# Performance work log

Hardware: AMD Instinct MI355X
Metric: run time of the kernel (lower is better)

The kernel has to match this reference:

```python
import jax, jax.numpy as jnp
import numpy as np

B, L, D, C, NB = 2, 256, 3, 256, 64
LN_EPS = 1e-5


def setup_inputs() -> dict:
    ks = jax.random.split(jax.random.key(0), 12)
    x_BLD = jax.random.normal(ks[0], (B, L, D), dtype=jnp.float32) * 0.5
    c_BD = jax.random.normal(ks[1], (B, C), dtype=jnp.float32)
    embed_w = jax.random.normal(ks[2], (NB, C), dtype=jnp.float32) * 0.02
    pos_w = jax.random.normal(ks[3], (128, C), dtype=jnp.float32) * 0.02
    bins = jnp.linspace(0.0, 3.0, NB - 1, dtype=jnp.float32)
    ada_w = jax.random.normal(ks[4], (3 * C, C), dtype=jnp.float32) * (C ** -0.5)
    ada_b = jnp.zeros((3 * C,), dtype=jnp.float32)
    ln_g = jnp.ones((C,), dtype=jnp.float32)
    ln_b = jnp.zeros((C,), dtype=jnp.float32)
    fc1_w = jax.random.normal(ks[5], (4 * C, C), dtype=jnp.float32) * (C ** -0.5)
    fc1_b = jnp.zeros((4 * C,), dtype=jnp.float32)
    fc2_w = jax.random.normal(ks[6], (C, 4 * C), dtype=jnp.float32) * ((4 * C) ** -0.5)
    fc2_b = jnp.zeros((C,), dtype=jnp.float32)
    return {"x_BLD": x_BLD, "c_BD": c_BD, "embed_w": embed_w, "pos_w": pos_w,
            "bins": bins, "ada_w": ada_w, "ada_b": ada_b, "ln_g": ln_g,
            "ln_b": ln_b, "fc1_w": fc1_w, "fc1_b": fc1_b, "fc2_w": fc2_w,
            "fc2_b": fc2_b}


def reference(x_BLD, c_BD, embed_w, pos_w, bins, ada_w, ada_b, ln_g, ln_b,
              fc1_w, fc1_b, fc2_w, fc2_b):
    # pairwise squared distances: [B, L, L]
    d_BLL = jnp.sum((x_BLD[:, :, None, :] - x_BLD[:, None, :, :]) ** 2, axis=-1)
    # bucketize (torch.bucketize right=False == searchsorted side='left')
    idx_BLL = jnp.searchsorted(bins, d_BLL, side="left")
    # relative position embedding: [L, L, C]
    rel = jnp.arange(L)[:, None] - jnp.arange(L)[None, :]
    rel = jnp.clip(rel, -64, 63) + 64
    pos_LLD = pos_w[rel]
    # adaLN modulation from conditioning: SiLU -> Linear -> 3 chunks
    mod = jax.nn.silu(c_BD) @ ada_w.T + ada_b            # [B, 3C]
    shift, scale, gate = jnp.split(mod, 3, axis=-1)      # each [B, C]
    shift = shift[:, None, None, :]
    scale = scale[:, None, None, :]
    gate = gate[:, None, None, :]
    # embed + pos, affine modulate
    s = embed_w[idx_BLL] + pos_LLD[None]                 # [B, L, L, C]
    s = s * (1.0 + scale) + shift
    # LayerNorm over channel dim
    mu = jnp.mean(s, axis=-1, keepdims=True)
    var = jnp.mean((s - mu) ** 2, axis=-1, keepdims=True)
    h = (s - mu) * jax.lax.rsqrt(var + LN_EPS) * ln_g + ln_b
    # MLP: Linear -> GELU(exact) -> Linear
    h = jax.nn.gelu(h @ fc1_w.T + fc1_b, approximate=False)
    h = h @ fc2_w.T + fc2_b
    return s + gate * h
```

## Files before the change

### kernel.cpp

```cpp
#include <hip/hip_runtime.h>
#include <math.h>

#define Cn 256
#define Ln 256
#define Bn 2
#define H1 1024
#define NIDX 64
#define NREL 128
#define NCOMBO 16384
#define TROWS 32

typedef __attribute__((ext_vector_type(8))) short bf16x8;
typedef __attribute__((ext_vector_type(4))) float f32x4;
typedef unsigned int u32;

__device__ __forceinline__ float gelu_exact(float x) {
    return 0.5f * x * (1.0f + erff(x * 0.70710678118654752f));
}
__device__ __forceinline__ short f2bf(float f) {
    unsigned u = __float_as_uint(f);
    return (short)((u + 0x7fffu + ((u >> 16) & 1u)) >> 16);
}

__global__ __launch_bounds__(256) void mod_kernel(
    const float* __restrict__ c_BD, const float* __restrict__ ada_w,
    const float* __restrict__ ada_b, float* __restrict__ mod)
{
    int o = blockIdx.x * 256 + threadIdx.x;
    int b = o / (3 * Cn);
    int j = o - b * (3 * Cn);
    const float* crow = c_BD + b * Cn;
    const float* wrow = ada_w + (size_t)j * Cn;
    float acc = 0.f;
    for (int k = 0; k < Cn; k += 4) {
        float4 cv = *(const float4*)(crow + k);
        float4 wv = *(const float4*)(wrow + k);
        acc += (cv.x / (1.f + expf(-cv.x))) * wv.x;
        acc += (cv.y / (1.f + expf(-cv.y))) * wv.y;
        acc += (cv.z / (1.f + expf(-cv.z))) * wv.z;
        acc += (cv.w / (1.f + expf(-cv.w))) * wv.w;
    }
    mod[o] = acc + ada_b[j];
}

__global__ __launch_bounds__(256) void cvt2_kernel(
    const float* __restrict__ s1, const float* __restrict__ s2,
    short* __restrict__ d1, short* __restrict__ d2)
{
    const int N = Cn * H1;
    int i = (blockIdx.x * 256 + threadIdx.x) * 4;
    const float* s;
    short* d;
    if (i < N) { s = s1 + i; d = d1 + i; }
    else       { s = s2 + (i - N); d = d2 + (i - N); }
    float4 v = *(const float4*)s;
    short4 o;
    o.x = f2bf(v.x); o.y = f2bf(v.y); o.z = f2bf(v.z); o.w = f2bf(v.w);
    *(short4*)d = o;
}

__global__ __launch_bounds__(256, 4) void table_fused_kernel(
    const float* __restrict__ embed_w, const float* __restrict__ pos_w,
    const float* __restrict__ ln_g, const float* __restrict__ ln_b,
    const short* __restrict__ fc1bf, const float* __restrict__ fc1_b,
    const short* __restrict__ fc2bf, const float* __restrict__ fc2_b,
    const float* __restrict__ mod, float* __restrict__ table)
{
    __shared__ __align__(16) short h_lds[TROWS][264];
    __shared__ __align__(16) short g_lds[TROWS][264];

    const int tid  = threadIdx.x;
    const int wave = tid >> 6;
    const int lane = tid & 63;
    const int quad = lane >> 4;
    const int l15  = lane & 15;

    const int base = blockIdx.x * TROWS;
    const int b    = base >> 13;
    const int idx  = (base >> 7) & 63;
    const int rel0 = base & 127;

    const float* modb = mod + b * (3 * Cn);
    const float* erow = embed_w + (size_t)idx * Cn;

    {
        const int c0 = lane * 4;
        float4 ev = *(const float4*)(erow + c0);
        float4 sc = *(const float4*)(modb + Cn + c0);
        sc.x += 1.f; sc.y += 1.f; sc.z += 1.f; sc.w += 1.f;
        const float4 sh = *(const float4*)(modb + c0);
        const float4 lg = *(const float4*)(ln_g + c0);
        const float4 lb = *(const float4*)(ln_b + c0);
        #pragma unroll
        for (int r8 = 0; r8 < 8; ++r8) {
            const int rr = wave * 8 + r8;
            const float4 p = *(const float4*)(pos_w + (size_t)(rel0 + rr) * Cn + c0);
            float v0 = (ev.x + p.x) * sc.x + sh.x;
            float v1 = (ev.y + p.y) * sc.y + sh.y;
            float v2 = (ev.z + p.z) * sc.z + sh.z;
            float v3 = (ev.w + p.w) * sc.w + sh.w;
            float sum = v0 + v1 + v2 + v3;
            #pragma unroll
            for (int off = 32; off; off >>= 1) sum += __shfl_xor(sum, off, 64);
            const float mu = sum * (1.f / Cn);
            float t0 = v0 - mu, t1 = v1 - mu, t2 = v2 - mu, t3 = v3 - mu;
            float p2 = t0 * t0 + t1 * t1 + t2 * t2 + t3 * t3;
            #pragma unroll
            for (int off = 32; off; off >>= 1) p2 += __shfl_xor(p2, off, 64);
            const float rstd = rsqrtf(p2 * (1.f / Cn) + 1e-5f);
            short4 hq;
            hq.x = f2bf(t0 * rstd * lg.x + lb.x);
            hq.y = f2bf(t1 * rstd * lg.y + lb.y);
            hq.z = f2bf(t2 * rstd * lg.z + lb.z);
            hq.w = f2bf(t3 * rstd * lg.w + lb.w);
            *(short4*)(&h_lds[rr][c0]) = hq;
        }
    }
    __syncthreads();

    f32x4 acc2[2][4];
    #pragma unroll
    for (int mt = 0; mt < 2; ++mt)
        #pragma unroll
        for (int nt = 0; nt < 4; ++nt) acc2[mt][nt] = (f32x4){0.f, 0.f, 0.f, 0.f};

    for (int c = 0; c < 4; ++c) {
        f32x4 z[2][4];
        #pragma unroll
        for (int mt = 0; mt < 2; ++mt)
            #pragma unroll
            for (int nt = 0; nt < 4; ++nt) z[mt][nt] = (f32x4){0.f, 0.f, 0.f, 0.f};

        #pragma unroll
        for (int ks = 0; ks < 8; ++ks) {
            const int k0 = ks * 32 + quad * 8;
            bf16x8 a0 = *(const bf16x8*)(&h_lds[l15][k0]);
            bf16x8 a1 = *(const bf16x8*)(&h_lds[16 + l15][k0]);
            #pragma unroll
            for (int nt = 0; nt < 4; ++nt) {
                const int n = c * 256 + wave * 64 + nt * 16 + l15;
                bf16x8 w = *(const bf16x8*)(fc1bf + (size_t)n * Cn + k0);
                z[0][nt] = __builtin_amdgcn_mfma_f32_16x16x32_bf16(w, a0, z[0][nt], 0, 0, 0);
                z[1][nt] = __builtin_amdgcn_mfma_f32_16x16x32_bf16(w, a1, z[1][nt], 0, 0, 0);
            }
        }
        __syncthreads();

        #pragma unroll
        for (int mt = 0; mt < 2; ++mt) {
            #pragma unroll
            for (int nt = 0; nt < 4; ++nt) {
                const int cc = wave * 64 + nt * 16 + quad * 4;
                const float4 b4 = *(const float4*)(fc1_b + c * 256 + cc);
                short4 o;
                o.x = f2bf(gelu_exact(z[mt][nt][0] + b4.x));
                o.y = f2bf(gelu_exact(z[mt][nt][1] + b4.y));
                o.z = f2bf(gelu_exact(z[mt][nt][2] + b4.z));
                o.w = f2bf(gelu_exact(z[mt][nt][3] + b4.w));
                *(short4*)(&g_lds[mt * 16 + l15][cc]) = o;
            }
        }
        __syncthreads();

        #pragma unroll
        for (int ks = 0; ks < 8; ++ks) {
            const int k0 = ks * 32 + quad * 8;
            bf16x8 a0 = *(const bf16x8*)(&g_lds[l15][k0]);
            bf16x8 a1 = *(const bf16x8*)(&g_lds[16 + l15][k0]);
            #pragma unroll
            for (int nt = 0; nt < 4; ++nt) {
                const int n = wave * 64 + nt * 16 + l15;
                bf16x8 w = *(const bf16x8*)(fc2bf + (size_t)n * H1 + c * 256 + k0);
                acc2[0][nt] = __builtin_amdgcn_mfma_f32_16x16x32_bf16(w, a0, acc2[0][nt], 0, 0, 0);
                acc2[1][nt] = __builtin_amdgcn_mfma_f32_16x16x32_bf16(w, a1, acc2[1][nt], 0, 0, 0);
            }
        }
    }

    #pragma unroll
    for (int mt = 0; mt < 2; ++mt) {
        const int row = mt * 16 + l15;
        const float* prow = pos_w + (size_t)(rel0 + row) * Cn;
        #pragma unroll
        for (int nt = 0; nt < 4; ++nt) {
            const int n0 = wave * 64 + nt * 16 + quad * 4;
            const float4 b4 = *(const float4*)(fc2_b + n0);
            const float4 g4 = *(const float4*)(modb + 2 * Cn + n0);
            const float4 sc = *(const float4*)(modb + Cn + n0);
            const float4 sh = *(const float4*)(modb + n0);
            const float4 e4 = *(const float4*)(erow + n0);
            const float4 p4 = *(const float4*)(prow + n0);
            float4 o;
            float s;
            s   = (e4.x + p4.x) * (1.f + sc.x) + sh.x;
            o.x = s + g4.x * (acc2[mt][nt][0] + b4.x);
            s   = (e4.y + p4.y) * (1.f + sc.y) + sh.y;
            o.y = s + g4.y * (acc2[mt][nt][1] + b4.y);
            s   = (e4.z + p4.z) * (1.f + sc.z) + sh.z;
            o.z = s + g4.z * (acc2[mt][nt][2] + b4.z);
            s   = (e4.w + p4.w) * (1.f + sc.w) + sh.w;
            o.w = s + g4.w * (acc2[mt][nt][3] + b4.w);
            *(float4*)(table + (size_t)(base + row) * Cn + n0) = o;
        }
    }
}

__global__ __launch_bounds__(256) void gather_kernel(
    const float* __restrict__ x, const float* __restrict__ bins,
    const float* __restrict__ table, float* __restrict__ out)
{
    __shared__ float xs[Ln * 3];
    __shared__ float bins_s[63];
    __shared__ int   idx_s[64];

    const int tid = threadIdx.x;
    const int blk = blockIdx.x;
    const int q   = blk & 3;
    const int bi  = blk >> 2;
    const int b   = bi >> 8;
    const int i   = bi & 255;

    for (int t = tid; t < Ln * 3; t += 256) xs[t] = x[(size_t)b * Ln * 3 + t];
    if (tid < 63) bins_s[tid] = bins[tid];
    __syncthreads();

    if (tid < 64) {
        int j = q * 64 + tid;
        float d0 = xs[3 * i]     - xs[3 * j];
        float d1 = xs[3 * i + 1] - xs[3 * j + 1];
        float d2 = xs[3 * i + 2] - xs[3 * j + 2];
        float d = d0 * d0 + d1 * d1 + d2 * d2;
        int v = 0;
        #pragma unroll
        for (int k = 0; k < 63; ++k) v += (bins_s[k] < d) ? 1 : 0;
        idx_s[tid] = v;
    }
    __syncthreads();

    const int wave = tid >> 6;
    const int lane = tid & 63;
    float4* outp = (float4*)(out + (size_t)bi * Ln * Cn);
    const float4* tab4 = (const float4*)table;

    float4 v[16];
    #pragma unroll
    for (int jj = 0; jj < 16; ++jj) {
        int jl  = wave * 16 + jj;
        int j   = q * 64 + jl;
        int rel = i - j;
        rel = (rel < -64 ? -64 : (rel > 63 ? 63 : rel)) + 64;
        size_t trow = (size_t)((b * NIDX + idx_s[jl]) * NREL + rel) * (Cn / 4);
        v[jj] = tab4[trow + lane];
    }
    #pragma unroll
    for (int jj = 0; jj < 16; ++jj) {
        int j = q * 64 + wave * 16 + jj;
        outp[(size_t)j * (Cn / 4) + lane] = v[jj];
    }
}

extern "C" void kernel_launch(void* const* d_in, const int* in_sizes, int n_in,
                              void* d_out, int out_size, void* d_ws, size_t ws_size,
                              hipStream_t stream) {
    const float* x_BLD   = (const float*)d_in[0];
    const float* c_BD    = (const float*)d_in[1];
    const float* embed_w = (const float*)d_in[2];
    const float* pos_w   = (const float*)d_in[3];
    const float* bins    = (const float*)d_in[4];
    const float* ada_w   = (const float*)d_in[5];
    const float* ada_b   = (const float*)d_in[6];
    const float* ln_g    = (const float*)d_in[7];
    const float* ln_b    = (const float*)d_in[8];
    const float* fc1_w   = (const float*)d_in[9];
    const float* fc1_b   = (const float*)d_in[10];
    const float* fc2_w   = (const float*)d_in[11];
    const float* fc2_b   = (const float*)d_in[12];
    float* out = (float*)d_out;

    char* ws = (char*)d_ws;
    float* mod   = (float*)ws;
    short* fc1bf = (short*)(ws + 8192);
    short* fc2bf = (short*)(ws + 8192 + 524288);
    float* table = (float*)(ws + 8192 + 2 * 524288);

    mod_kernel<<<(Bn * 3 * Cn) / 256, 256, 0, stream>>>(c_BD, ada_w, ada_b, mod);
    cvt2_kernel<<<2 * Cn * H1 / 4 / 256, 256, 0, stream>>>(fc1_w, fc2_w, fc1bf, fc2bf);
    table_fused_kernel<<<NCOMBO / TROWS, 256, 0, stream>>>(
        embed_w, pos_w, ln_g, ln_b, fc1bf, fc1_b, fc2bf, fc2_b, mod, table);
    gather_kernel<<<Bn * Ln * 4, 256, 0, stream>>>(x_BLD, bins, table, out);
}
```

Before: 279.9 us.

## Merge prep kernels, double table kernel waves, and prefetch MFMA weights into registers

Merges the adaLN modulation and bf16 weight conversion into one prep launch, removing a kernel launch. The table kernel now runs 512 threads (8 waves) per block, with each wave owning 32 output columns instead of 64. All fc1/fc2 weight fragments for a chunk are loaded into registers before the MFMA loop, so global loads overlap instead of being interleaved with compute. The last barrier is skipped on the final chunk. This raises register pressure from the prefetched fragments, and the launch bound of 512 threads with 4 blocks per CU may limit occupancy or cause spills.

```diff
diff --git a/kernel.cpp b/kernel.cpp
--- a/kernel.cpp
+++ b/kernel.cpp
@@ -22,44 +22,45 @@
     return (short)((u + 0x7fffu + ((u >> 16) & 1u)) >> 16);
 }
 
-__global__ __launch_bounds__(256) void mod_kernel(
+__global__ __launch_bounds__(256) void prep_kernel(
     const float* __restrict__ c_BD, const float* __restrict__ ada_w,
-    const float* __restrict__ ada_b, float* __restrict__ mod)
+    const float* __restrict__ ada_b, const float* __restrict__ fc1_w,
+    const float* __restrict__ fc2_w, float* __restrict__ mod,
+    short* __restrict__ fc1bf, short* __restrict__ fc2bf)
 {
-    int o = blockIdx.x * 256 + threadIdx.x;
-    int b = o / (3 * Cn);
-    int j = o - b * (3 * Cn);
-    const float* crow = c_BD + b * Cn;
-    const float* wrow = ada_w + (size_t)j * Cn;
-    float acc = 0.f;
-    for (int k = 0; k < Cn; k += 4) {
-        float4 cv = *(const float4*)(crow + k);
-        float4 wv = *(const float4*)(wrow + k);
-        acc += (cv.x / (1.f + expf(-cv.x))) * wv.x;
-        acc += (cv.y / (1.f + expf(-cv.y))) * wv.y;
-        acc += (cv.z / (1.f + expf(-cv.z))) * wv.z;
-        acc += (cv.w / (1.f + expf(-cv.w))) * wv.w;
-    }
-    mod[o] = acc + ada_b[j];
-}
-
-__global__ __launch_bounds__(256) void cvt2_kernel(
-    const float* __restrict__ s1, const float* __restrict__ s2,
-    short* __restrict__ d1, short* __restrict__ d2)
-{
-    const int N = Cn * H1;
-    int i = (blockIdx.x * 256 + threadIdx.x) * 4;
-    const float* s;
-    short* d;
-    if (i < N) { s = s1 + i; d = d1 + i; }
-    else       { s = s2 + (i - N); d = d2 + (i - N); }
-    float4 v = *(const float4*)s;
-    short4 o;
-    o.x = f2bf(v.x); o.y = f2bf(v.y); o.z = f2bf(v.z); o.w = f2bf(v.w);
-    *(short4*)d = o;
-}
-
-__global__ __launch_bounds__(256, 4) void table_fused_kernel(
+    const int bid = blockIdx.x;
+    const int tid = threadIdx.x;
+    if (bid < 512) {
+        const int N = Cn * H1;
+        int i = (bid * 256 + tid) * 4;
+        const float* s;
+        short* d;
+        if (i < N) { s = fc1_w + i; d = fc1bf + i; }
+        else       { s = fc2_w + (i - N); d = fc2bf + (i - N); }
+        float4 v = *(const float4*)s;
+        short4 o;
+        o.x = f2bf(v.x); o.y = f2bf(v.y); o.z = f2bf(v.z); o.w = f2bf(v.w);
+        *(short4*)d = o;
+    } else {
+        int o = (bid - 512) * 256 + tid;
+        int b = o / (3 * Cn);
+        int j = o - b * (3 * Cn);
+        const float* crow = c_BD + b * Cn;
+        const float* wrow = ada_w + (size_t)j * Cn;
+        float acc = 0.f;
+        for (int k = 0; k < Cn; k += 4) {
+            float4 cv = *(const float4*)(crow + k);
+            float4 wv = *(const float4*)(wrow + k);
+            acc += (cv.x / (1.f + expf(-cv.x))) * wv.x;
+            acc += (cv.y / (1.f + expf(-cv.y))) * wv.y;
+            acc += (cv.z / (1.f + expf(-cv.z))) * wv.z;
+            acc += (cv.w / (1.f + expf(-cv.w))) * wv.w;
+        }
+        mod[o] = acc + ada_b[j];
+    }
+}
+
+__global__ __launch_bounds__(512, 4) void table_fused_kernel(
     const float* __restrict__ embed_w, const float* __restrict__ pos_w,
     const float* __restrict__ ln_g, const float* __restrict__ ln_b,
     const short* __restrict__ fc1bf, const float* __restrict__ fc1_b,
@@ -92,8 +93,8 @@
         const float4 lg = *(const float4*)(ln_g + c0);
         const float4 lb = *(const float4*)(ln_b + c0);
         #pragma unroll
-        for (int r8 = 0; r8 < 8; ++r8) {
-            const int rr = wave * 8 + r8;
+        for (int r4 = 0; r4 < 4; ++r4) {
+            const int rr = wave * 4 + r4;
             const float4 p = *(const float4*)(pos_w + (size_t)(rel0 + rr) * Cn + c0);
             float v0 = (ev.x + p.x) * sc.x + sh.x;
             float v1 = (ev.y + p.y) * sc.y + sh.y;
@@ -118,30 +119,53 @@
     }
     __syncthreads();
 
-    f32x4 acc2[2][4];
+    f32x4 acc2[2][2];
     #pragma unroll
     for (int mt = 0; mt < 2; ++mt)
         #pragma unroll
-        for (int nt = 0; nt < 4; ++nt) acc2[mt][nt] = (f32x4){0.f, 0.f, 0.f, 0.f};
+        for (int nt = 0; nt < 2; ++nt) acc2[mt][nt] = (f32x4){0.f, 0.f, 0.f, 0.f};
 
     for (int c = 0; c < 4; ++c) {
-        f32x4 z[2][4];
+        f32x4 z[2][2];
         #pragma unroll
         for (int mt = 0; mt < 2; ++mt)
             #pragma unroll
-            for (int nt = 0; nt < 4; ++nt) z[mt][nt] = (f32x4){0.f, 0.f, 0.f, 0.f};
-
-        #pragma unroll
-        for (int ks = 0; ks < 8; ++ks) {
-            const int k0 = ks * 32 + quad * 8;
-            bf16x8 a0 = *(const bf16x8*)(&h_lds[l15][k0]);
-            bf16x8 a1 = *(const bf16x8*)(&h_lds[16 + l15][k0]);
-            #pragma unroll
-            for (int nt = 0; nt < 4; ++nt) {
-                const int n = c * 256 + wave * 64 + nt * 16 + l15;
-                bf16x8 w = *(const bf16x8*)(fc1bf + (size_t)n * Cn + k0);
-                z[0][nt] = __builtin_amdgcn_mfma_f32_16x16x32_bf16(w, a0, z[0][nt], 0, 0, 0);
-                z[1][nt] = __builtin_amdgcn_mfma_f32_16x16x32_bf16(w, a1, z[1][nt], 0, 0, 0);
+            for (int nt = 0; nt < 2; ++nt) z[mt][nt] = (f32x4){0.f, 0.f, 0.f, 0.f};
+
+        {
+            const short* w1base = fc1bf + (size_t)(c * 256 + wave * 32 + l15) * Cn + quad * 8;
+            bf16x8 wA[4][2], wB[4][2];
+            #pragma unroll
+            for (int ks = 0; ks < 4; ++ks)
+                #pragma unroll
+                for (int nt = 0; nt < 2; ++nt)
+                    wA[ks][nt] = *(const bf16x8*)(w1base + nt * 16 * Cn + ks * 32);
+            #pragma unroll
+            for (int ks = 0; ks < 4; ++ks)
+                #pragma unroll
+                for (int nt = 0; nt < 2; ++nt)
+                    wB[ks][nt] = *(const bf16x8*)(w1base + nt * 16 * Cn + (ks + 4) * 32);
+            #pragma unroll
+            for (int ks = 0; ks < 4; ++ks) {
+                const int k0 = ks * 32 + quad * 8;
+                bf16x8 a0 = *(const bf16x8*)(&h_lds[l15][k0]);
+                bf16x8 a1 = *(const bf16x8*)(&h_lds[16 + l15][k0]);
+                #pragma unroll
+                for (int nt = 0; nt < 2; ++nt) {
+                    z[0][nt] = __builtin_amdgcn_mfma_f32_16x16x32_bf16(wA[ks][nt], a0, z[0][nt], 0, 0, 0);
+                    z[1][nt] = __builtin_amdgcn_mfma_f32_16x16x32_bf16(wA[ks][nt], a1, z[1][nt], 0, 0, 0);
+                }
+            }
+            #pragma unroll
+            for (int ks = 0; ks < 4; ++ks) {
+                const int k0 = (ks + 4) * 32 + quad * 8;
+                bf16x8 a0 = *(const bf16x8*)(&h_lds[l15][k0]);
+                bf16x8 a1 = *(const bf16x8*)(&h_lds[16 + l15][k0]);
+                #pragma unroll
+                for (int nt = 0; nt < 2; ++nt) {
+                    z[0][nt] = __builtin_amdgcn_mfma_f32_16x16x32_bf16(wB[ks][nt], a0, z[0][nt], 0, 0, 0);
+                    z[1][nt] = __builtin_amdgcn_mfma_f32_16x16x32_bf16(wB[ks][nt], a1, z[1][nt], 0, 0, 0);
+                }
             }
         }
         __syncthreads();
@@ -149,8 +173,8 @@
         #pragma unroll
         for (int mt = 0; mt < 2; ++mt) {
             #pragma unroll
-            for (int nt = 0; nt < 4; ++nt) {
-                const int cc = wave * 64 + nt * 16 + quad * 4;
+            for (int nt = 0; nt < 2; ++nt) {
+                const int cc = wave * 32 + nt * 16 + quad * 4;
                 const float4 b4 = *(const float4*)(fc1_b + c * 256 + cc);
                 short4 o;
                 o.x = f2bf(gelu_exact(z[mt][nt][0] + b4.x));
@@ -162,19 +186,43 @@
         }
         __syncthreads();
 
-        #pragma unroll
-        for (int ks = 0; ks < 8; ++ks) {
-            const int k0 = ks * 32 + quad * 8;
-            bf16x8 a0 = *(const bf16x8*)(&g_lds[l15][k0]);
-            bf16x8 a1 = *(const bf16x8*)(&g_lds[16 + l15][k0]);
-            #pragma unroll
-            for (int nt = 0; nt < 4; ++nt) {
-                const int n = wave * 64 + nt * 16 + l15;
-                bf16x8 w = *(const bf16x8*)(fc2bf + (size_t)n * H1 + c * 256 + k0);
-                acc2[0][nt] = __builtin_amdgcn_mfma_f32_16x16x32_bf16(w, a0, acc2[0][nt], 0, 0, 0);
-                acc2[1][nt] = __builtin_amdgcn_mfma_f32_16x16x32_bf16(w, a1, acc2[1][nt], 0, 0, 0);
-            }
-        }
+        {
+            const short* w2base = fc2bf + (size_t)(wave * 32 + l15) * H1 + c * 256 + quad * 8;
+            bf16x8 wA[4][2], wB[4][2];
+            #pragma unroll
+            for (int ks = 0; ks < 4; ++ks)
+                #pragma unroll
+                for (int nt = 0; nt < 2; ++nt)
+                    wA[ks][nt] = *(const bf16x8*)(w2base + nt * 16 * H1 + ks * 32);
+            #pragma unroll
+            for (int ks = 0; ks < 4; ++ks)
+                #pragma unroll
+                for (int nt = 0; nt < 2; ++nt)
+                    wB[ks][nt] = *(const bf16x8*)(w2base + nt * 16 * H1 + (ks + 4) * 32);
+            #pragma unroll
+            for (int ks = 0; ks < 4; ++ks) {
+                const int k0 = ks * 32 + quad * 8;
+                bf16x8 a0 = *(const bf16x8*)(&g_lds[l15][k0]);
+                bf16x8 a1 = *(const bf16x8*)(&g_lds[16 + l15][k0]);
+                #pragma unroll
+                for (int nt = 0; nt < 2; ++nt) {
+                    acc2[0][nt] = __builtin_amdgcn_mfma_f32_16x16x32_bf16(wA[ks][nt], a0, acc2[0][nt], 0, 0, 0);
+                    acc2[1][nt] = __builtin_amdgcn_mfma_f32_16x16x32_bf16(wA[ks][nt], a1, acc2[1][nt], 0, 0, 0);
+                }
+            }
+            #pragma unroll
+            for (int ks = 0; ks < 4; ++ks) {
+                const int k0 = (ks + 4) * 32 + quad * 8;
+                bf16x8 a0 = *(const bf16x8*)(&g_lds[l15][k0]);
+                bf16x8 a1 = *(const bf16x8*)(&g_lds[16 + l15][k0]);
+                #pragma unroll
+                for (int nt = 0; nt < 2; ++nt) {
+                    acc2[0][nt] = __builtin_amdgcn_mfma_f32_16x16x32_bf16(wB[ks][nt], a0, acc2[0][nt], 0, 0, 0);
+                    acc2[1][nt] = __builtin_amdgcn_mfma_f32_16x16x32_bf16(wB[ks][nt], a1, acc2[1][nt], 0, 0, 0);
+                }
+            }
+        }
+        if (c < 3) __syncthreads();
     }
 
     #pragma unroll
@@ -182,8 +230,8 @@
         const int row = mt * 16 + l15;
         const float* prow = pos_w + (size_t)(rel0 + row) * Cn;
         #pragma unroll
-        for (int nt = 0; nt < 4; ++nt) {
-            const int n0 = wave * 64 + nt * 16 + quad * 4;
+        for (int nt = 0; nt < 2; ++nt) {
+            const int n0 = wave * 32 + nt * 16 + quad * 4;
             const float4 b4 = *(const float4*)(fc2_b + n0);
             const float4 g4 = *(const float4*)(modb + 2 * Cn + n0);
             const float4 sc = *(const float4*)(modb + Cn + n0);
@@ -283,9 +331,9 @@
     short* fc2bf = (short*)(ws + 8192 + 524288);
     float* table = (float*)(ws + 8192 + 2 * 524288);
 
-    mod_kernel<<<(Bn * 3 * Cn) / 256, 256, 0, stream>>>(c_BD, ada_w, ada_b, mod);
-    cvt2_kernel<<<2 * Cn * H1 / 4 / 256, 256, 0, stream>>>(fc1_w, fc2_w, fc1bf, fc2bf);
-    table_fused_kernel<<<NCOMBO / TROWS, 256, 0, stream>>>(
+    prep_kernel<<<518, 256, 0, stream>>>(c_BD, ada_w, ada_b, fc1_w, fc2_w,
+                                         mod, fc1bf, fc2bf);
+    table_fused_kernel<<<NCOMBO / TROWS, 512, 0, stream>>>(
         embed_w, pos_w, ln_g, ln_b, fc1bf, fc1_b, fc2bf, fc2_b, mod, table);
     gather_kernel<<<Bn * Ln * 4, 256, 0, stream>>>(x_BLD, bins, table, out);
 }
```

After: 268.6 us. -4.0%, faster.
